# Performance work log

Measured on AMD Instinct MI355X. Metric: run time of the kernel, lower is better.

Reference implementation:

```python
import jax, jax.numpy as jnp
import numpy as np

B, NPIX, M, N_CP, N_CA = 8, 256, 8192, 24576, 24576
EPS = 1e-16


def setup_inputs() -> dict:
    key = jax.random.key(0)
    k1, k2, k3, k4, k5, k6 = jax.random.split(key, 6)
    images = jax.random.normal(k1, (B, NPIX, NPIX), dtype=jnp.float32)
    # k-space trajectory in radians/pixel, range [-pi, pi) as torchkbnufft expects
    ktraj = (jax.random.uniform(k2, (2, M), dtype=jnp.float32) * 2.0 - 1.0) * np.float32(np.pi)
    pulsefac = jax.random.normal(k3, (2, M), dtype=jnp.float32)
    cphase_sign = jnp.sign(jax.random.normal(k4, (3, N_CP), dtype=jnp.float32))
    cphase_ind = jax.random.randint(k5, (3, N_CP), 0, M, dtype=jnp.int32)
    camp_ind = jax.random.randint(k6, (4, N_CA), 0, M, dtype=jnp.int32)
    return {"images": images, "ktraj": ktraj, "pulsefac": pulsefac,
            "cphase_sign": cphase_sign, "cphase_ind": cphase_ind, "camp_ind": camp_ind}


def reference(images, ktraj, pulsefac, cphase_sign, cphase_ind, camp_ind):
    npix = images.shape[-1]
    # centered image coordinates (Fessler NUFFT convention, n_shift = npix//2)
    coords = (jnp.arange(npix) - npix // 2).astype(jnp.float32)
    kv, ku = ktraj[0], ktraj[1]  # (M,) each
    # separable exact NDFT: exp(-i(kv*y + ku*x)) = Ev[m,y] * Eu[m,x]
    Ev = jnp.exp(-1j * kv[:, None] * coords[None, :]).astype(jnp.complex64)  # (M, npix)
    Eu = jnp.exp(-1j * ku[:, None] * coords[None, :]).astype(jnp.complex64)  # (M, npix)
    img_c = images.astype(jnp.complex64)
    tmp = jnp.einsum('byx,my->bmx', img_c, Ev)        # (B, M, npix)
    kdata = jnp.einsum('bmx,mx->bm', tmp, Eu)          # (B, M) complex visibilities
    # pulse-function correction (complex multiply)
    pf = pulsefac[0] + 1j * pulsefac[1]                # (M,)
    vis_c = kdata * pf                                 # (B, M)
    vis = jnp.stack([vis_c.real, vis_c.imag], axis=1)  # (B, 2, M)
    visamp = jnp.sqrt(vis_c.real ** 2 + vis_c.imag ** 2 + EPS)  # (B, M)
    # closure phases: gather triangle visibilities, signed phase sum, degrees
    v_tri = vis_c[:, cphase_ind]                       # (B, 3, N_cp)
    ang = jnp.arctan2(v_tri.imag, v_tri.real)          # (B, 3, N_cp)
    cphase = jnp.einsum('kn,bkn->bn', cphase_sign, ang) * np.float32(180.0 / np.pi)
    # log closure amplitudes: gather quadrangle visibilities
    v_quad = vis_c[:, camp_ind]                        # (B, 4, N_ca)
    amp = jnp.sqrt(v_quad.real ** 2 + v_quad.imag ** 2 + EPS)
    logcamp = (jnp.log(amp[:, 0]) + jnp.log(amp[:, 1])
               - jnp.log(amp[:, 2]) - jnp.log(amp[:, 3]))  # (B, N_ca)
    return vis, visamp, cphase, logcamp
```

## Files before the change

kernel.cpp:

```cpp
#include <hip/hip_runtime.h>
#include <cmath>

#define BB   8
#define NPIX 256
#define MM   8192
#define NCP  24576
#define NCA  24576
#define EPSF 1e-16f

#define KC   32
#define TMB  64

#define VIS_OFF    0
#define VISAMP_OFF (BB * 2 * MM)
#define CPH_OFF    (VISAMP_OFF + BB * MM)
#define LCA_OFF    (CPH_OFF + BB * NCP)

typedef __bf16 bf16x8 __attribute__((ext_vector_type(8)));
typedef float  f32x4  __attribute__((ext_vector_type(4)));

#define WIDX(row, k8) (((row) >> 4) * 512 + (k8) * 128 + ((row) & 15) * 8)

__global__ __launch_bounds__(256, 2)
void nufft_vis_mfma(const float* __restrict__ images,
                    const float* __restrict__ ktraj,
                    const float* __restrict__ pulsefac,
                    float* __restrict__ out)
{
    __shared__ __align__(16) __bf16 sArh[TMB * KC];
    __shared__ __align__(16) __bf16 sArl[TMB * KC];
    __shared__ __align__(16) __bf16 sAih[TMB * KC];
    __shared__ __align__(16) __bf16 sAil[TMB * KC];
    __shared__ __align__(16) __bf16 sBh[NPIX * KC];
    __shared__ __align__(16) __bf16 sBl[NPIX * KC];

    const int tid  = threadIdx.x;
    const int m0   = blockIdx.x * TMB;
    const int b    = blockIdx.y;
    const int lane = tid & 63;
    const int w    = tid >> 6;
    const int ln15 = lane & 15;
    const int q    = lane >> 4;

    const float kvm = ktraj[m0 + lane];
    float rots, rotc;
    sincosf(kvm, &rots, &rotc);
    const float* imgb = images + b * NPIX * NPIX + tid;
    const int ao = WIDX(lane, w);

    f32x4 acc[2][16];
    #pragma unroll
    for (int rt = 0; rt < 2; ++rt)
        #pragma unroll
        for (int ct = 0; ct < 16; ++ct)
            acc[rt][ct] = (f32x4){0.f, 0.f, 0.f, 0.f};

    for (int y0 = 0; y0 < NPIX; y0 += KC) {
        {
            float s, c;
            sincosf(kvm * (float)(y0 + w * 8 - 128), &s, &c);
            float er = c, ei = -s;
            bf16x8 vrh, vrl, vih, vil;
            #pragma unroll
            for (int j = 0; j < 8; ++j) {
                __bf16 h = (__bf16)er;
                vrh[j] = h; vrl[j] = (__bf16)(er - (float)h);
                h = (__bf16)ei;
                vih[j] = h; vil[j] = (__bf16)(ei - (float)h);
                const float nr = er * rotc + ei * rots;
                const float ni = ei * rotc - er * rots;
                er = nr; ei = ni;
            }
            *(bf16x8*)&sArh[ao] = vrh;
            *(bf16x8*)&sArl[ao] = vrl;
            *(bf16x8*)&sAih[ao] = vih;
            *(bf16x8*)&sAil[ao] = vil;
        }
        #pragma unroll
        for (int gg = 0; gg < 4; ++gg) {
            bf16x8 bh, bl;
            #pragma unroll
            for (int j = 0; j < 8; ++j) {
                const float v = imgb[(y0 + gg * 8 + j) * NPIX];
                const __bf16 h = (__bf16)v;
                bh[j] = h; bl[j] = (__bf16)(v - (float)h);
            }
            const int bo = WIDX(tid, gg);
            *(bf16x8*)&sBh[bo] = bh;
            *(bf16x8*)&sBl[bo] = bl;
        }
        __syncthreads();

        const int aro = WIDX(w * 16 + ln15, q);
        const bf16x8 ah0 = *(const bf16x8*)&sArh[aro];
        const bf16x8 al0 = *(const bf16x8*)&sArl[aro];
        const bf16x8 ah1 = *(const bf16x8*)&sAih[aro];
        const bf16x8 al1 = *(const bf16x8*)&sAil[aro];

        #pragma unroll
        for (int ct = 0; ct < 16; ++ct) {
            const int bro = WIDX(ct * 16 + ln15, q);
            const bf16x8 bh = *(const bf16x8*)&sBh[bro];
            const bf16x8 bl = *(const bf16x8*)&sBl[bro];
            acc[0][ct] = __builtin_amdgcn_mfma_f32_16x16x32_bf16(ah0, bh, acc[0][ct], 0, 0, 0);
            acc[0][ct] = __builtin_amdgcn_mfma_f32_16x16x32_bf16(ah0, bl, acc[0][ct], 0, 0, 0);
            acc[0][ct] = __builtin_amdgcn_mfma_f32_16x16x32_bf16(al0, bh, acc[0][ct], 0, 0, 0);
            acc[1][ct] = __builtin_amdgcn_mfma_f32_16x16x32_bf16(ah1, bh, acc[1][ct], 0, 0, 0);
            acc[1][ct] = __builtin_amdgcn_mfma_f32_16x16x32_bf16(ah1, bl, acc[1][ct], 0, 0, 0);
            acc[1][ct] = __builtin_amdgcn_mfma_f32_16x16x32_bf16(al1, bh, acc[1][ct], 0, 0, 0);
        }
        __syncthreads();
    }

    #pragma unroll
    for (int r = 0; r < 4; ++r) {
        const int m = m0 + w * 16 + q * 4 + r;
        const float ku = ktraj[MM + m];
        float s0, c0, s16, c16;
        sincosf(ku * (float)(ln15 - 128), &s0, &c0);
        sincosf(ku * 16.0f, &s16, &c16);
        float er = c0, ei = -s0;
        float sr = 0.f, si = 0.f;
        #pragma unroll
        for (int ct = 0; ct < 16; ++ct) {
            const float tr = acc[0][ct][r];
            const float ti = acc[1][ct][r];
            sr = fmaf(tr, er, fmaf(-ti, ei, sr));
            si = fmaf(tr, ei, fmaf(ti, er, si));
            const float nr = er * c16 + ei * s16;
            const float ni = ei * c16 - er * s16;
            er = nr; ei = ni;
        }
        #pragma unroll
        for (int off = 8; off >= 1; off >>= 1) {
            sr += __shfl_xor(sr, off);
            si += __shfl_xor(si, off);
        }
        if (ln15 == 0) {
            const float pr = pulsefac[m];
            const float pi = pulsefac[MM + m];
            const float vr = sr * pr - si * pi;
            const float vi = sr * pi + si * pr;
            out[b * 2 * MM + m]      = vr;
            out[b * 2 * MM + MM + m] = vi;
            out[VISAMP_OFF + b * MM + m] = sqrtf(vr * vr + vi * vi + EPSF);
        }
    }
}

__global__ void gather_fused(const float* __restrict__ vis,
                             const float* __restrict__ sign,
                             const int* __restrict__ cind,
                             const int* __restrict__ caind,
                             float* __restrict__ out)
{
    const int i = blockIdx.x * 256 + threadIdx.x;
    if (i >= BB * NCP) return;
    const int b = i / NCP;
    const int n = i - b * NCP;
    const float* vb = vis + b * 2 * MM;

    float cp = 0.f;
    #pragma unroll
    for (int k = 0; k < 3; ++k) {
        const int m = cind[k * NCP + n];
        cp += sign[k * NCP + n] * atan2f(vb[MM + m], vb[m]);
    }
    out[CPH_OFF + i] = cp * 57.29577951308232f;

    float p[4];
    #pragma unroll
    for (int k = 0; k < 4; ++k) {
        const int m = caind[k * NCA + n];
        const float vr = vb[m];
        const float vi = vb[MM + m];
        p[k] = vr * vr + vi * vi + EPSF;
    }
    out[LCA_OFF + i] = 0.5f * __logf((p[0] * p[1]) / (p[2] * p[3]));
}

extern "C" void kernel_launch(void* const* d_in, const int* in_sizes, int n_in,
                              void* d_out, int out_size, void* d_ws, size_t ws_size,
                              hipStream_t stream)
{
    const float* images   = (const float*)d_in[0];
    const float* ktraj    = (const float*)d_in[1];
    const float* pulsefac = (const float*)d_in[2];
    const float* csign    = (const float*)d_in[3];
    const int*   cind     = (const int*)d_in[4];
    const int*   caind    = (const int*)d_in[5];
    float* out = (float*)d_out;

    dim3 grid(MM / TMB, BB);
    nufft_vis_mfma<<<grid, 256, 0, stream>>>(images, ktraj, pulsefac, out);
    gather_fused<<<(BB * NCP + 255) / 256, 256, 0, stream>>>(out, csign, cind, caind, out);
}
```

Baseline: 122.8 us.

## Double M-tile per block to 128 rows with 512 threads; use polynomial atan2

Each NUFFT block now covers 128 k-space samples with 8 waves instead of 64 with 4. The image tile staged in LDS is shared by twice as many rows, which halves the redundant image loads and bf16 splitting per output. Thread roles for building the A and B tiles are remapped to fit the larger block, and launch bounds go to 512 threads with 4 blocks, which tightens the register budget on a 32-accumulator kernel. The gather kernel also swaps atan2f for a minimax polynomial approximation, trading some accuracy for fewer instructions.

```diff
diff --git a/kernel.cpp b/kernel.cpp
--- a/kernel.cpp
+++ b/kernel.cpp
@@ -9,7 +9,8 @@
 #define EPSF 1e-16f
 
 #define KC   32
-#define TMB  64
+#define TMB  128
+#define NT   512
 
 #define VIS_OFF    0
 #define VISAMP_OFF (BB * 2 * MM)
@@ -21,7 +22,7 @@
 
 #define WIDX(row, k8) (((row) >> 4) * 512 + (k8) * 128 + ((row) & 15) * 8)
 
-__global__ __launch_bounds__(256, 2)
+__global__ __launch_bounds__(NT, 4)
 void nufft_vis_mfma(const float* __restrict__ images,
                     const float* __restrict__ ktraj,
                     const float* __restrict__ pulsefac,
@@ -42,11 +43,16 @@
     const int ln15 = lane & 15;
     const int q    = lane >> 4;
 
-    const float kvm = ktraj[m0 + lane];
+    const int arow = tid & 127;
+    const int aoct = tid >> 7;
+    const float kvm = ktraj[m0 + arow];
     float rots, rotc;
     sincosf(kvm, &rots, &rotc);
-    const float* imgb = images + b * NPIX * NPIX + tid;
-    const int ao = WIDX(lane, w);
+    const int ao = WIDX(arow, aoct);
+
+    const int bx    = tid & 255;
+    const int bhalf = tid >> 8;
+    const float* imgb = images + b * NPIX * NPIX + bx;
 
     f32x4 acc[2][16];
     #pragma unroll
@@ -58,7 +64,7 @@
     for (int y0 = 0; y0 < NPIX; y0 += KC) {
         {
             float s, c;
-            sincosf(kvm * (float)(y0 + w * 8 - 128), &s, &c);
+            sincosf(kvm * (float)(y0 + aoct * 8 - 128), &s, &c);
             float er = c, ei = -s;
             bf16x8 vrh, vrl, vih, vil;
             #pragma unroll
@@ -77,15 +83,16 @@
             *(bf16x8*)&sAil[ao] = vil;
         }
         #pragma unroll
-        for (int gg = 0; gg < 4; ++gg) {
+        for (int oo = 0; oo < 2; ++oo) {
+            const int oct = bhalf * 2 + oo;
             bf16x8 bh, bl;
             #pragma unroll
             for (int j = 0; j < 8; ++j) {
-                const float v = imgb[(y0 + gg * 8 + j) * NPIX];
+                const float v = imgb[(y0 + oct * 8 + j) * NPIX];
                 const __bf16 h = (__bf16)v;
                 bh[j] = h; bl[j] = (__bf16)(v - (float)h);
             }
-            const int bo = WIDX(tid, gg);
+            const int bo = WIDX(bx, oct);
             *(bf16x8*)&sBh[bo] = bh;
             *(bf16x8*)&sBl[bo] = bl;
         }
@@ -148,6 +155,23 @@
     }
 }
 
+__device__ __forceinline__ float fast_atan2f(float y, float x)
+{
+    const float ax = fabsf(x), ay = fabsf(y);
+    const float mx = fmaxf(ax, ay), mn = fminf(ax, ay);
+    const float a  = mn / fmaxf(mx, 1e-37f);
+    const float s  = a * a;
+    float r = 0.0208351f;
+    r = fmaf(r, s, -0.0851330f);
+    r = fmaf(r, s,  0.1801410f);
+    r = fmaf(r, s, -0.3302995f);
+    r = fmaf(r, s,  0.9998660f);
+    r *= a;
+    r = (ay > ax) ? (1.57079632679f - r) : r;
+    r = (x < 0.0f) ? (3.14159265359f - r) : r;
+    return (y < 0.0f) ? -r : r;
+}
+
 __global__ void gather_fused(const float* __restrict__ vis,
                              const float* __restrict__ sign,
                              const int* __restrict__ cind,
@@ -164,7 +188,7 @@
     #pragma unroll
     for (int k = 0; k < 3; ++k) {
         const int m = cind[k * NCP + n];
-        cp += sign[k * NCP + n] * atan2f(vb[MM + m], vb[m]);
+        cp += sign[k * NCP + n] * fast_atan2f(vb[MM + m], vb[m]);
     }
     out[CPH_OFF + i] = cp * 57.29577951308232f;
 
@@ -192,6 +216,6 @@
     float* out = (float*)d_out;
 
     dim3 grid(MM / TMB, BB);
-    nufft_vis_mfma<<<grid, 256, 0, stream>>>(images, ktraj, pulsefac, out);
+    nufft_vis_mfma<<<grid, NT, 0, stream>>>(images, ktraj, pulsefac, out);
     gather_fused<<<(BB * NCP + 255) / 256, 256, 0, stream>>>(out, csign, cind, caind, out);
 }
```

Result: slower. 241.1 us (+96.4%).
